# Optimization experiments

Measured on AMD Instinct MI355X. Metric: run time of the kernel, lower is better.

The kernel has to match this reference:

```python
import jax, jax.numpy as jnp
import numpy as np

STRIDE = 1
PAD = 1
DIL = 1


def setup_inputs() -> dict:
    key = jax.random.key(0)
    k1, k2, k3, k4 = jax.random.split(key, 4)
    N, Cin, H, W = 4, 256, 64, 64
    Cout, kh, kw = 256, 3, 3
    inputs = jax.random.normal(k1, (N, Cin, H, W), jnp.float32)
    filter = jax.random.normal(k2, (Cout, Cin, kh, kw), jnp.float32) * 0.05
    # offsets in pixels (y,x interleaved per tap), typical magnitude O(1)
    offset = jax.random.normal(k3, (N, 2 * kh * kw, H, W), jnp.float32)
    # modulation mask in [0,1) (post-sigmoid in real nets)
    mask = jax.random.uniform(k4, (N, kh * kw, H, W), jnp.float32)
    return {"inputs": inputs, "filter": filter, "offset": offset, "mask": mask}


def _dcn_forward(inputs, filt, offset, mask):
    N, C, H, W = inputs.shape
    Cout, _, kh, kw = filt.shape
    K = kh * kw
    Ho = (H + 2 * PAD - DIL * (kh - 1) - 1) // STRIDE + 1
    Wo = (W + 2 * PAD - DIL * (kw - 1) - 1) // STRIDE + 1

    # base sampling grid per kernel tap: [K, Ho, Wo]
    ki, kj = jnp.meshgrid(jnp.arange(kh), jnp.arange(kw), indexing='ij')
    ki = ki.reshape(K, 1, 1)
    kj = kj.reshape(K, 1, 1)
    base_y = (jnp.arange(Ho)[None, :, None] * STRIDE - PAD + ki * DIL).astype(jnp.float32)
    base_x = (jnp.arange(Wo)[None, None, :] * STRIDE - PAD + kj * DIL).astype(jnp.float32)

    # offset channels: per tap k, channel 2k = dy, channel 2k+1 = dx
    off = offset.reshape(N, K, 2, Ho, Wo)
    y = base_y[None] + off[:, :, 0]  # [N, K, Ho, Wo]
    x = base_x[None] + off[:, :, 1]

    y0 = jnp.floor(y)
    x0 = jnp.floor(x)
    ly = y - y0  # fractional parts, [N, K, Ho, Wo]
    lx = x - x0
    y0i = y0.astype(jnp.int32)
    x0i = x0.astype(jnp.int32)

    def gather(img, yy, xx):
        # img [C,H,W]; yy,xx [K,Ho,Wo] int; zero outside bounds
        valid = (yy >= 0) & (yy < H) & (xx >= 0) & (xx < W)
        yc = jnp.clip(yy, 0, H - 1)
        xc = jnp.clip(xx, 0, W - 1)
        return img[:, yc, xc] * valid.astype(img.dtype)  # [C,K,Ho,Wo]

    def sample_one(img, y0i, x0i, ly, lx):
        v00 = gather(img, y0i, x0i)
        v01 = gather(img, y0i, x0i + 1)
        v10 = gather(img, y0i + 1, x0i)
        v11 = gather(img, y0i + 1, x0i + 1)
        return (v00 * (1 - ly) * (1 - lx) + v01 * (1 - ly) * lx
                + v10 * ly * (1 - lx) + v11 * ly * lx)

    # bilinear-sampled, modulated im2col columns: [N, C, K, Ho, Wo]
    col = jax.vmap(sample_one)(inputs, y0i, x0i, ly, lx)
    col = col * mask.reshape(N, 1, K, Ho, Wo)

    # grouped conv with num_groups=1: plain GEMM over (C, K)
    out = jnp.einsum('ock,nckhw->nohw', filt.reshape(Cout, C, K), col)
    return out


def reference(inputs, filter, offset, mask):
    return _dcn_forward(inputs, filter, offset, mask)
```

## Files before the change

kernel.cpp:

```cpp
#include <hip/hip_runtime.h>
#include <stdint.h>

typedef __attribute__((ext_vector_type(4))) float f32x4;
typedef __attribute__((ext_vector_type(8))) short bf16x8;

static constexpr int N_ = 4, C_ = 256, HW_ = 4096;
static constexpr int CO_ = 256, KTAP = 9, KK = 2304;
static constexpr int NSTEP = 72;
static constexpr int A_STEP_BYTES = 16 * 64 * 16;

static constexpr size_t NHWC_BYTES = (size_t)N_ * HW_ * C_ * 2;
static constexpr size_t ABF_OFF    = NHWC_BYTES;
static constexpr size_t ABF_BYTES  = (size_t)NSTEP * A_STEP_BYTES;

__device__ inline unsigned f2bf(float f) {
  unsigned u = __builtin_bit_cast(unsigned, f);
  unsigned r = u + 0x7FFFu + ((u >> 16) & 1u);
  return r >> 16;
}
__device__ inline float asf(unsigned u) { return __builtin_bit_cast(float, u); }

__global__ __launch_bounds__(256) void k_nchw_to_nhwc(const float* __restrict__ in,
                                                      unsigned short* __restrict__ nhwc) {
  __shared__ float tile[64][65];
  int b = blockIdx.x;
  int n = b >> 8, cg = (b >> 6) & 3, hwg = b & 63;
  int c0 = cg * 64, hw0 = hwg * 64;
  int t = threadIdx.x;
  int col = t & 63, r0 = t >> 6;
  const float* src = in + (size_t)(n * C_ + c0) * HW_ + hw0;
#pragma unroll
  for (int i = 0; i < 16; ++i) {
    int row = r0 + i * 4;
    tile[row][col] = src[(size_t)row * HW_ + col];
  }
  __syncthreads();
  int pr = t >> 2, cc0 = (t & 3) * 16;
  unsigned us[8];
#pragma unroll
  for (int i = 0; i < 8; ++i) {
    unsigned lo = f2bf(tile[cc0 + 2 * i][pr]);
    unsigned hi = f2bf(tile[cc0 + 2 * i + 1][pr]);
    us[i] = lo | (hi << 16);
  }
  unsigned* dst = (unsigned*)(nhwc + (size_t)(n * HW_ + hw0 + pr) * C_ + c0 + cc0);
  ((uint4*)dst)[0] = make_uint4(us[0], us[1], us[2], us[3]);
  ((uint4*)dst)[1] = make_uint4(us[4], us[5], us[6], us[7]);
}

__global__ __launch_bounds__(256) void k_prep_filter(const float* __restrict__ filt,
                                                     unsigned short* __restrict__ abf2) {
  int gid = blockIdx.x * 256 + threadIdx.x;
  int o = gid >> 8, c = gid & 255;
  const float* f = filt + (size_t)(o * C_ + c) * KTAP;
  int rb = o >> 4;
  int lane = ((c >> 3) & 3) * 16 + (o & 15);
  int j = c & 7;
#pragma unroll
  for (int tap = 0; tap < KTAP; ++tap) {
    int s = tap * 8 + (c >> 5);
    abf2[((size_t)(s * 16 + rb) * 64 + lane) * 8 + j] = (unsigned short)f2bf(f[tap]);
  }
}

struct GB { unsigned g[4]; f32x4 w; };

__device__ __forceinline__ void buildB2(const unsigned* g, f32x4 w, char* dst) {
  float r0 = w.x * asf(g[0] << 16) + w.y * asf(g[1] << 16) +
             w.z * asf(g[2] << 16) + w.w * asf(g[3] << 16);
  float r1 = w.x * asf(g[0] & 0xffff0000u) + w.y * asf(g[1] & 0xffff0000u) +
             w.z * asf(g[2] & 0xffff0000u) + w.w * asf(g[3] & 0xffff0000u);
  *(unsigned*)dst = f2bf(r0) | (f2bf(r1) << 16);
}

#define MFMA_BF16 __builtin_amdgcn_mfma_f32_16x16x32_bf16

#define PIPE(S, GCON, GISS, ACUR, ANXT, RDP, WRP)                                 \
  do {                                                                            \
    int s1_ = (S) + 1 < NSTEP ? (S) + 1 : NSTEP - 1;                              \
    int s2_ = (S) + 2 < NSTEP ? (S) + 2 : NSTEP - 1;                              \
    ANXT = *(const bf16x8*)(aoff + (size_t)s1_ * A_STEP_BYTES);                   \
    if ((s2_ & 7) == 0) {                                                         \
      int tp_ = s2_ >> 3;                                                         \
      raS = *(const uint4*)&recA[(tp_ * 64 + p_b) * 4];                           \
      wS  = *(const f32x4*)&recW[(tp_ * 64 + p_b) * 4];                           \
    }                                                                             \
    {                                                                             \
      unsigned co_ = (unsigned)((s2_ & 7) * 64);                                  \
      GISS.g[0] = *(const unsigned*)(nb_t + raS.x + co_);                         \
      GISS.g[1] = *(const unsigned*)(nb_t + raS.y + co_);                         \
      GISS.g[2] = *(const unsigned*)(nb_t + raS.z + co_);                         \
      GISS.g[3] = *(const unsigned*)(nb_t + raS.w + co_);                         \
      GISS.w = wS;                                                                \
    }                                                                             \
    __builtin_amdgcn_sched_barrier(0);                                            \
    {                                                                             \
      const char* bb_ = (const char*)&Bl[0][0] + (RDP) * 4096;                    \
      bf16x8 b0_ = *(const bf16x8*)(bb_ + bo0);                                   \
      bf16x8 b1_ = *(const bf16x8*)(bb_ + bo1);                                   \
      bf16x8 b2_ = *(const bf16x8*)(bb_ + bo2);                                   \
      bf16x8 b3_ = *(const bf16x8*)(bb_ + bo3);                                   \
      __builtin_amdgcn_s_setprio(1);                                              \
      acc[0] = MFMA_BF16(ACUR, b0_, acc[0], 0, 0, 0);                             \
      acc[1] = MFMA_BF16(ACUR, b1_, acc[1], 0, 0, 0);                             \
      acc[2] = MFMA_BF16(ACUR, b2_, acc[2], 0, 0, 0);                             \
      acc[3] = MFMA_BF16(ACUR, b3_, acc[3], 0, 0, 0);                             \
      __builtin_amdgcn_s_setprio(0);                                              \
    }                                                                             \
    buildB2(GCON.g, GCON.w, (WRP) ? bw1 : bw0);                                   \
    asm volatile("s_waitcnt lgkmcnt(0)" ::: "memory");                            \
    __builtin_amdgcn_s_barrier();                                                 \
    asm volatile("" ::: "memory");                                                \
  } while (0)

__global__ __launch_bounds__(1024, 4) void k_dcn_gemm(const unsigned short* __restrict__ nhwc,
                                                      const unsigned short* __restrict__ abf2,
                                                      const float* __restrict__ offs,
                                                      const float* __restrict__ msk,
                                                      float* __restrict__ out) {
  __shared__ __align__(16) unsigned short Bl[2][2048];
  __shared__ float recW[KTAP * 64 * 4];
  __shared__ unsigned recA[KTAP * 64 * 4];

  int bid = blockIdx.x;
  int b = ((bid & 7) << 5) | (bid >> 3);
  int n = b >> 6;
  int ho = b & 63;
  int hw0 = ho << 6;
  int t = threadIdx.x;

  for (int r = t; r < 576; r += 1024) {
    int pl = r / 9;
    int tap = r - pl * 9;
    int hw = hw0 + pl;
    float dy = offs[(size_t)(n * 18 + 2 * tap) * HW_ + hw];
    float dx = offs[(size_t)(n * 18 + 2 * tap + 1) * HW_ + hw];
    float mk = msk[(size_t)(n * 9 + tap) * HW_ + hw];
    float y = (float)(ho - 1 + tap / 3) + dy;
    float x = (float)(pl - 1 + tap % 3) + dx;
    float fy = floorf(y), fx = floorf(x);
    float ly = y - fy, lx = x - fx;
    int y0 = (int)fy, x0 = (int)fx;
    int y1 = y0 + 1, x1 = x0 + 1;
    float vy0 = (y0 >= 0 && y0 < 64) ? 1.f : 0.f;
    float vy1 = (y1 >= 0 && y1 < 64) ? 1.f : 0.f;
    float vx0 = (x0 >= 0 && x0 < 64) ? 1.f : 0.f;
    float vx1 = (x1 >= 0 && x1 < 64) ? 1.f : 0.f;
    int y0c = min(max(y0, 0), 63), y1c = min(max(y1, 0), 63);
    int x0c = min(max(x0, 0), 63), x1c = min(max(x1, 0), 63);
    int base = (tap * 64 + pl) * 4;
    recW[base + 0] = (1.f - ly) * (1.f - lx) * mk * vy0 * vx0;
    recW[base + 1] = (1.f - ly) * lx * mk * vy0 * vx1;
    recW[base + 2] = ly * (1.f - lx) * mk * vy1 * vx0;
    recW[base + 3] = ly * lx * mk * vy1 * vx1;
    recA[base + 0] = (unsigned)((y0c * 64 + x0c) * 512);
    recA[base + 1] = (unsigned)((y0c * 64 + x1c) * 512);
    recA[base + 2] = (unsigned)((y1c * 64 + x0c) * 512);
    recA[base + 3] = (unsigned)((y1c * 64 + x1c) * 512);
  }
  __syncthreads();

  int lane = t & 63, wv = t >> 6;
  int p_b = t >> 4;
  int cg = t & 15;
  int cq = cg >> 2, ck = cg & 3;

  const char* aoff = (const char*)abf2 + ((size_t)(wv * 64 + lane)) * 16;
  const char* nb_t = (const char*)nhwc + (size_t)n * HW_ * C_ * 2 + cg * 4;
  int wbyte = cq * 1024 + (((p_b + 4 * cq) & 63) * 16) + ck * 4;
  char* bw0 = (char*)&Bl[0][0] + wbyte;
  char* bw1 = (char*)&Bl[0][0] + 4096 + wbyte;

  int cqr = lane >> 4;
  int rslot = (lane & 15) + 4 * cqr;
  const int bo0 = cqr * 1024 + ((rslot + 0) & 63) * 16;
  const int bo1 = cqr * 1024 + ((rslot + 16) & 63) * 16;
  const int bo2 = cqr * 1024 + ((rslot + 32) & 63) * 16;
  const int bo3 = cqr * 1024 + ((rslot + 48) & 63) * 16;

  f32x4 acc[4];
#pragma unroll
  for (int ni = 0; ni < 4; ++ni) acc[ni] = (f32x4){0.f, 0.f, 0.f, 0.f};

  GB gA, gB;
  bf16x8 afc, afn;
  uint4 raS;
  f32x4 wS;

  raS = *(const uint4*)&recA[p_b * 4];
  wS  = *(const f32x4*)&recW[p_b * 4];
  gA.g[0] = *(const unsigned*)(nb_t + raS.x);
  gA.g[1] = *(const unsigned*)(nb_t + raS.y);
  gA.g[2] = *(const unsigned*)(nb_t + raS.z);
  gA.g[3] = *(const unsigned*)(nb_t + raS.w);
  gA.w = wS;
  gB.g[0] = *(const unsigned*)(nb_t + raS.x + 64);
  gB.g[1] = *(const unsigned*)(nb_t + raS.y + 64);
  gB.g[2] = *(const unsigned*)(nb_t + raS.z + 64);
  gB.g[3] = *(const unsigned*)(nb_t + raS.w + 64);
  gB.w = wS;
  afc = *(const bf16x8*)(aoff);
  buildB2(gA.g, gA.w, bw0);
  asm volatile("s_waitcnt lgkmcnt(0)" ::: "memory");
  __builtin_amdgcn_s_barrier();
  asm volatile("" ::: "memory");

  for (int s = 0; s < NSTEP; s += 2) {
    PIPE(s,     gB, gA, afc, afn, 0, 1);
    PIPE(s + 1, gA, gB, afn, afc, 1, 0);
  }

  float* ob = out + (size_t)n * CO_ * HW_ + hw0;
#pragma unroll
  for (int ni = 0; ni < 4; ++ni)
#pragma unroll
    for (int j = 0; j < 4; ++j) {
      int o = wv * 16 + (lane >> 4) * 4 + j;
      int hw = ni * 16 + (lane & 15);
      ob[(size_t)o * HW_ + hw] = acc[ni][j];
    }
}

extern "C" void kernel_launch(void* const* d_in, const int* in_sizes, int n_in,
                              void* d_out, int out_size, void* d_ws, size_t ws_size,
                              hipStream_t stream) {
  const float* inp  = (const float*)d_in[0];
  const float* filt = (const float*)d_in[1];
  const float* offs = (const float*)d_in[2];
  const float* msk  = (const float*)d_in[3];
  float* out = (float*)d_out;
  if (ws_size < ABF_OFF + ABF_BYTES) return;
  unsigned short* nhwc = (unsigned short*)d_ws;
  unsigned short* abf2 = (unsigned short*)((char*)d_ws + ABF_OFF);

  k_nchw_to_nhwc<<<1024, 256, 0, stream>>>(inp, nhwc);
  k_prep_filter<<<256, 256, 0, stream>>>(filt, abf2);
  k_dcn_gemm<<<256, 1024, 0, stream>>>(nhwc, abf2, offs, msk, out);
}
```

Measured before the change: 56.48 us.

## Retile GEMM waves to 2x2 MFMA blocks with XOR LDS swizzle and packed bf16 convert

Each wave now computes a 32-output-channel by 32-pixel tile as a 2x2 grid of MFMAs instead of 16 channels by 64 pixels. Each wave therefore reads two A fragments and two B fragments per step rather than one A and four B, which lowers LDS read traffic per MFMA. The LDS layout changes from a rotate-by-offset swizzle to an XOR swizzle. The bilinear blend now uses packed two-wide float math and the hardware v_cvt_pk_bf16_f32 instruction, and the per-lane channel offset is folded into the gather base addresses. In exchange, the wave holds twice as many A-fragment registers and does twice as many global A loads.

New measurement: 58.69 us. +3.9%, slower.

```diff
diff --git a/kernel.cpp b/kernel.cpp
--- a/kernel.cpp
+++ b/kernel.cpp
@@ -1,6 +1,7 @@
 #include <hip/hip_runtime.h>
 #include <stdint.h>
 
+typedef __attribute__((ext_vector_type(2))) float f32x2;
 typedef __attribute__((ext_vector_type(4))) float f32x4;
 typedef __attribute__((ext_vector_type(8))) short bf16x8;
 
@@ -66,31 +67,37 @@
 struct GB { unsigned g[4]; f32x4 w; };
 
 __device__ __forceinline__ void buildB2(const unsigned* g, f32x4 w, char* dst) {
-  float r0 = w.x * asf(g[0] << 16) + w.y * asf(g[1] << 16) +
-             w.z * asf(g[2] << 16) + w.w * asf(g[3] << 16);
-  float r1 = w.x * asf(g[0] & 0xffff0000u) + w.y * asf(g[1] & 0xffff0000u) +
-             w.z * asf(g[2] & 0xffff0000u) + w.w * asf(g[3] & 0xffff0000u);
-  *(unsigned*)dst = f2bf(r0) | (f2bf(r1) << 16);
+  f32x2 a0 = {asf(g[0] << 16), asf(g[0] & 0xffff0000u)};
+  f32x2 a1 = {asf(g[1] << 16), asf(g[1] & 0xffff0000u)};
+  f32x2 a2 = {asf(g[2] << 16), asf(g[2] & 0xffff0000u)};
+  f32x2 a3 = {asf(g[3] << 16), asf(g[3] & 0xffff0000u)};
+  f32x2 r = w.x * a0 + w.y * a1 + w.z * a2 + w.w * a3;
+  unsigned o;
+  asm("v_cvt_pk_bf16_f32 %0, %1, %2" : "=v"(o) : "v"(r.x), "v"(r.y));
+  *(unsigned*)dst = o;
 }
 
 #define MFMA_BF16 __builtin_amdgcn_mfma_f32_16x16x32_bf16
 
-#define PIPE(S, GCON, GISS, ACUR, ANXT, RDP, WRP)                                 \
+#define PIPE(S, GCON, GISS, AC0, AC1, AN0, AN1, RDP, WRP)                         \
   do {                                                                            \
     int s1_ = (S) + 1 < NSTEP ? (S) + 1 : NSTEP - 1;                              \
     int s2_ = (S) + 2 < NSTEP ? (S) + 2 : NSTEP - 1;                              \
-    ANXT = *(const bf16x8*)(aoff + (size_t)s1_ * A_STEP_BYTES);                   \
+    AN0 = *(const bf16x8*)(aoff0 + (size_t)s1_ * A_STEP_BYTES);                   \
+    AN1 = *(const bf16x8*)(aoff1 + (size_t)s1_ * A_STEP_BYTES);                   \
     if ((s2_ & 7) == 0) {                                                         \
       int tp_ = s2_ >> 3;                                                         \
-      raS = *(const uint4*)&recA[(tp_ * 64 + p_b) * 4];                           \
-      wS  = *(const f32x4*)&recW[(tp_ * 64 + p_b) * 4];                           \
+      uint4 ra_ = *(const uint4*)&recA[(tp_ * 64 + p_b) * 4];                     \
+      wS = *(const f32x4*)&recW[(tp_ * 64 + p_b) * 4];                            \
+      vS.x = ra_.x + cg4; vS.y = ra_.y + cg4;                                     \
+      vS.z = ra_.z + cg4; vS.w = ra_.w + cg4;                                     \
     }                                                                             \
     {                                                                             \
       unsigned co_ = (unsigned)((s2_ & 7) * 64);                                  \
-      GISS.g[0] = *(const unsigned*)(nb_t + raS.x + co_);                         \
-      GISS.g[1] = *(const unsigned*)(nb_t + raS.y + co_);                         \
-      GISS.g[2] = *(const unsigned*)(nb_t + raS.z + co_);                         \
-      GISS.g[3] = *(const unsigned*)(nb_t + raS.w + co_);                         \
+      GISS.g[0] = *(const unsigned*)(nb_u + vS.x + co_);                          \
+      GISS.g[1] = *(const unsigned*)(nb_u + vS.y + co_);                          \
+      GISS.g[2] = *(const unsigned*)(nb_u + vS.z + co_);                          \
+      GISS.g[3] = *(const unsigned*)(nb_u + vS.w + co_);                          \
       GISS.w = wS;                                                                \
     }                                                                             \
     __builtin_amdgcn_sched_barrier(0);                                            \
@@ -98,13 +105,11 @@
       const char* bb_ = (const char*)&Bl[0][0] + (RDP) * 4096;                    \
       bf16x8 b0_ = *(const bf16x8*)(bb_ + bo0);                                   \
       bf16x8 b1_ = *(const bf16x8*)(bb_ + bo1);                                   \
-      bf16x8 b2_ = *(const bf16x8*)(bb_ + bo2);                                   \
-      bf16x8 b3_ = *(const bf16x8*)(bb_ + bo3);                                   \
       __builtin_amdgcn_s_setprio(1);                                              \
-      acc[0] = MFMA_BF16(ACUR, b0_, acc[0], 0, 0, 0);                             \
-      acc[1] = MFMA_BF16(ACUR, b1_, acc[1], 0, 0, 0);                             \
-      acc[2] = MFMA_BF16(ACUR, b2_, acc[2], 0, 0, 0);                             \
-      acc[3] = MFMA_BF16(ACUR, b3_, acc[3], 0, 0, 0);                             \
+      acc[0][0] = MFMA_BF16(AC0, b0_, acc[0][0], 0, 0, 0);                        \
+      acc[1][0] = MFMA_BF16(AC1, b0_, acc[1][0], 0, 0, 0);                        \
+      acc[0][1] = MFMA_BF16(AC0, b1_, acc[0][1], 0, 0, 0);                        \
+      acc[1][1] = MFMA_BF16(AC1, b1_, acc[1][1], 0, 0, 0);                        \
       __builtin_amdgcn_s_setprio(0);                                              \
     }                                                                             \
     buildB2(GCON.g, GCON.w, (WRP) ? bw1 : bw0);                                   \
@@ -161,64 +166,75 @@
   __syncthreads();
 
   int lane = t & 63, wv = t >> 6;
+  int ig = wv >> 1;
+  int jg = wv & 1;
   int p_b = t >> 4;
   int cg = t & 15;
   int cq = cg >> 2, ck = cg & 3;
-
-  const char* aoff = (const char*)abf2 + ((size_t)(wv * 64 + lane)) * 16;
-  const char* nb_t = (const char*)nhwc + (size_t)n * HW_ * C_ * 2 + cg * 4;
-  int wbyte = cq * 1024 + (((p_b + 4 * cq) & 63) * 16) + ck * 4;
+  unsigned cg4 = (unsigned)(cg * 4);
+
+  const char* aoff0 = (const char*)abf2 + ((ig * 2 + 0) * 64 + lane) * 16;
+  const char* aoff1 = (const char*)abf2 + ((ig * 2 + 1) * 64 + lane) * 16;
+  const char* nb_u = (const char*)nhwc + (size_t)n * HW_ * C_ * 2;
+
+  int wbyte = cq * 1024 + ((p_b ^ (4 * cq)) * 16) + ck * 4;
   char* bw0 = (char*)&Bl[0][0] + wbyte;
-  char* bw1 = (char*)&Bl[0][0] + 4096 + wbyte;
-
-  int cqr = lane >> 4;
-  int rslot = (lane & 15) + 4 * cqr;
-  const int bo0 = cqr * 1024 + ((rslot + 0) & 63) * 16;
-  const int bo1 = cqr * 1024 + ((rslot + 16) & 63) * 16;
-  const int bo2 = cqr * 1024 + ((rslot + 32) & 63) * 16;
-  const int bo3 = cqr * 1024 + ((rslot + 48) & 63) * 16;
-
-  f32x4 acc[4];
-#pragma unroll
-  for (int ni = 0; ni < 4; ++ni) acc[ni] = (f32x4){0.f, 0.f, 0.f, 0.f};
+  char* bw1 = bw0 + 4096;
+
+  int c_r = lane >> 4;
+  int pxl0 = jg * 32 + (lane & 15);
+  const int bo0 = c_r * 1024 + ((pxl0 ^ (4 * c_r)) * 16);
+  const int bo1 = c_r * 1024 + (((pxl0 + 16) ^ (4 * c_r)) * 16);
+
+  f32x4 acc[2][2];
+#pragma unroll
+  for (int mi = 0; mi < 2; ++mi)
+#pragma unroll
+    for (int ni = 0; ni < 2; ++ni) acc[mi][ni] = (f32x4){0.f, 0.f, 0.f, 0.f};
 
   GB gA, gB;
-  bf16x8 afc, afn;
-  uint4 raS;
+  bf16x8 afc0, afc1, afn0, afn1;
+  uint4 vS;
   f32x4 wS;
 
-  raS = *(const uint4*)&recA[p_b * 4];
-  wS  = *(const f32x4*)&recW[p_b * 4];
-  gA.g[0] = *(const unsigned*)(nb_t + raS.x);
-  gA.g[1] = *(const unsigned*)(nb_t + raS.y);
-  gA.g[2] = *(const unsigned*)(nb_t + raS.z);
-  gA.g[3] = *(const unsigned*)(nb_t + raS.w);
-  gA.w = wS;
-  gB.g[0] = *(const unsigned*)(nb_t + raS.x + 64);
-  gB.g[1] = *(const unsigned*)(nb_t + raS.y + 64);
-  gB.g[2] = *(const unsigned*)(nb_t + raS.z + 64);
-  gB.g[3] = *(const unsigned*)(nb_t + raS.w + 64);
-  gB.w = wS;
-  afc = *(const bf16x8*)(aoff);
-  buildB2(gA.g, gA.w, bw0);
-  asm volatile("s_waitcnt lgkmcnt(0)" ::: "memory");
-  __builtin_amdgcn_s_barrier();
-  asm volatile("" ::: "memory");
+  {
+    uint4 ra0 = *(const uint4*)&recA[p_b * 4];
+    wS = *(const f32x4*)&recW[p_b * 4];
+    vS.x = ra0.x + cg4; vS.y = ra0.y + cg4; vS.z = ra0.z + cg4; vS.w = ra0.w + cg4;
+    gA.g[0] = *(const unsigned*)(nb_u + vS.x);
+    gA.g[1] = *(const unsigned*)(nb_u + vS.y);
+    gA.g[2] = *(const unsigned*)(nb_u + vS.z);
+    gA.g[3] = *(const unsigned*)(nb_u + vS.w);
+    gA.w = wS;
+    gB.g[0] = *(const unsigned*)(nb_u + vS.x + 64);
+    gB.g[1] = *(const unsigned*)(nb_u + vS.y + 64);
+    gB.g[2] = *(const unsigned*)(nb_u + vS.z + 64);
+    gB.g[3] = *(const unsigned*)(nb_u + vS.w + 64);
+    gB.w = wS;
+    afc0 = *(const bf16x8*)(aoff0);
+    afc1 = *(const bf16x8*)(aoff1);
+    buildB2(gA.g, gA.w, bw0);
+    asm volatile("s_waitcnt lgkmcnt(0)" ::: "memory");
+    __builtin_amdgcn_s_barrier();
+    asm volatile("" ::: "memory");
+  }
 
   for (int s = 0; s < NSTEP; s += 2) {
-    PIPE(s,     gB, gA, afc, afn, 0, 1);
-    PIPE(s + 1, gA, gB, afn, afc, 1, 0);
-  }
-
-  float* ob = out + (size_t)n * CO_ * HW_ + hw0;
-#pragma unroll
-  for (int ni = 0; ni < 4; ++ni)
-#pragma unroll
-    for (int j = 0; j < 4; ++j) {
-      int o = wv * 16 + (lane >> 4) * 4 + j;
-      int hw = ni * 16 + (lane & 15);
-      ob[(size_t)o * HW_ + hw] = acc[ni][j];
-    }
+    PIPE(s,     gB, gA, afc0, afc1, afn0, afn1, 0, 1);
+    PIPE(s + 1, gA, gB, afn0, afn1, afc0, afc1, 1, 0);
+  }
+
+  float* ob = out + (size_t)n * CO_ * HW_ + hw0 + jg * 32;
+#pragma unroll
+  for (int mi = 0; mi < 2; ++mi)
+#pragma unroll
+    for (int ni = 0; ni < 2; ++ni)
+#pragma unroll
+      for (int jj = 0; jj < 4; ++jj) {
+        int o = ig * 32 + mi * 16 + (lane >> 4) * 4 + jj;
+        int hw = ni * 16 + (lane & 15);
+        ob[(size_t)o * HW_ + hw] = acc[mi][ni][jj];
+      }
 }
 
 extern "C" void kernel_launch(void* const* d_in, const int* in_sizes, int n_in,
```
